# Kernel tuning notes

Measured on AMD Instinct MI355X. Metric: run time of the kernel, lower is better.

The kernel has to match this reference:

```python
import jax, jax.numpy as jnp
import numpy as np

FOCAL_ALPHA = 0.25
FOCAL_GAMMA = 2.0
LAMBDA_L1, LAMBDA_GIOU, LAMBDA_CONF = 1.0, 2.0, 1.0
IOU_THRESH = 0.3  # hardcoded `max_iou > 0.3` in assign_positives


def _make_boxes(key, shape):
    # valid xyxy boxes in [0,1]: random center + moderate size
    r = jax.random.uniform(key, shape + (4,), dtype=jnp.float32)
    cx = 0.1 + 0.8 * r[..., 0]
    cy = 0.1 + 0.8 * r[..., 1]
    w = 0.05 + 0.30 * r[..., 2]
    h = 0.05 + 0.30 * r[..., 3]
    return jnp.stack([cx - w / 2, cy - h / 2, cx + w / 2, cy + h / 2], axis=-1)


def setup_inputs() -> dict:
    key = jax.random.key(0)
    k1, k2, k3, k4, k5 = jax.random.split(key, 5)
    B, C, H, W, N = 16, 64, 80, 80, 32
    pred_boxes = _make_boxes(k1, (B, C, H, W))          # [B,C,H,W,4] xyxy
    confidences = jax.random.uniform(k2, (B, C, H, W), dtype=jnp.float32)
    cam = jax.random.uniform(k3, (B, C, H, W), dtype=jnp.float32)
    gt_boxes = _make_boxes(k4, (B, N))                   # [B,N,4] xyxy
    gt_labels = jax.random.randint(k5, (B, N), 0, C, dtype=jnp.int32)
    return {"pred_boxes": pred_boxes, "confidences": confidences, "cam": cam,
            "gt_boxes": gt_boxes, "gt_labels": gt_labels}


def box_giou(b1, b2):
    """Generalized IoU for xyxy boxes, broadcasting over leading dims."""
    a1 = (b1[..., 2] - b1[..., 0]) * (b1[..., 3] - b1[..., 1])
    a2 = (b2[..., 2] - b2[..., 0]) * (b2[..., 3] - b2[..., 1])
    lt = jnp.maximum(b1[..., :2], b2[..., :2])
    rb = jnp.minimum(b1[..., 2:], b2[..., 2:])
    wh = jnp.clip(rb - lt, 0.0)
    inter = wh[..., 0] * wh[..., 1]
    union = a1 + a2 - inter
    iou = inter / union
    lte = jnp.minimum(b1[..., :2], b2[..., :2])
    rbe = jnp.maximum(b1[..., 2:], b2[..., 2:])
    whe = jnp.clip(rbe - lte, 0.0)
    ae = whe[..., 0] * whe[..., 1]
    return iou - (ae - union) / ae


def _loss(pred_boxes, confidences, cam, gt_boxes, gt_labels):
    B, C, H, W, _ = pred_boxes.shape
    N = gt_boxes.shape[1]
    ii = jnp.arange(H)
    jj = jnp.arange(W)
    ch = jnp.arange(C)

    def assign_one(pb, gb, gl):  # pb [C,H,W,4], gb [N,4], gl [N]
        def step(carry, g):
            pos, matched = carry
            lab = gl[g]
            box = gb[g]
            pc = pb[lab].reshape(H * W, 4)
            giou = box_giou(pc, box[None, :])          # [H*W]
            idx = jnp.argmax(giou)
            valid = giou[idx] > IOU_THRESH
            mi, mj = idx // W, idx % W
            # pos_radius=1.5 -> window rows [mi-2, mi+1], cols [mj-2, mj+1]
            win = (((ii >= mi - 2) & (ii <= mi + 1))[:, None]
                   & ((jj >= mj - 2) & (jj <= mj + 1))[None, :])
            full = (ch == lab)[:, None, None] & (valid & win)[None]
            return (pos | full, jnp.where(full, g, matched)), None

        init = (jnp.zeros((C, H, W), bool), jnp.full((C, H, W), -1, jnp.int32))
        (pos, matched), _ = jax.lax.scan(step, init, jnp.arange(N))
        return pos, matched

    pos_mask, matched = jax.vmap(assign_one)(pred_boxes, gt_boxes, gt_labels)
    # gather matched gt box per position (later gts overwrite earlier, as in scan)
    gt_at = jax.vmap(lambda gb, m: gb[m])(gt_boxes, jnp.maximum(matched, 0))  # [B,C,H,W,4]

    l1 = jnp.mean(jnp.abs(pred_boxes - gt_at), axis=-1)   # F.l1_loss per pair
    giou_p = box_giou(pred_boxes, gt_at)
    num_pos = jnp.sum(pos_mask)
    denom = jnp.maximum(num_pos, 1).astype(jnp.float32)
    loss_l1 = jnp.sum(jnp.where(pos_mask, l1, 0.0)) / denom
    loss_giou = jnp.sum(jnp.where(pos_mask, 1.0 - giou_p, 0.0)) / denom

    conf_t = pos_mask.astype(jnp.float32)
    p = jnp.clip(confidences, 1e-6, 1.0 - 1e-6)
    ce = -(conf_t * jnp.log(p) + (1.0 - conf_t) * jnp.log1p(-p))
    p_t = p * conf_t + (1.0 - p) * (1.0 - conf_t)
    alpha_t = FOCAL_ALPHA * conf_t + (1.0 - FOCAL_ALPHA) * (1.0 - conf_t)
    loss_conf = jnp.mean(alpha_t * (1.0 - p_t) ** FOCAL_GAMMA * ce)

    loss_total = LAMBDA_L1 * loss_l1 + LAMBDA_GIOU * loss_giou + LAMBDA_CONF * loss_conf
    pos_ratio = num_pos.astype(jnp.float32) / (B * C * H * W)
    return loss_l1, loss_giou, loss_conf, loss_total, pos_ratio


@jax.jit
def reference(pred_boxes, confidences, cam, gt_boxes, gt_labels):
    return _loss(pred_boxes, confidences, cam, gt_boxes, gt_labels)
```

## Files before the change

### kernel.cpp

```cpp
#include <hip/hip_runtime.h>
#include <math.h>

constexpr int B = 16, C = 64, H = 80, Wd = 80, N = 32;
constexpr int HW = H * Wd;
constexpr int CHW = C * HW;
constexpr long long TOTAL = (long long)B * CHW;


constexpr int A_ITER = HW / 256;

__global__ __launch_bounds__(256) void assign_kernel(
    const float* __restrict__ pred,
    const float* __restrict__ gtb,
    const int*   __restrict__ gtl,
    int4* __restrict__ assign)
{
#pragma clang fp contract(off)
    const int bg = blockIdx.x;
    const int b = bg >> 5;
    const int g = bg & 31;
    const int tid = threadIdx.x;

    const int lab = gtl[b * N + g];
    const float4 gb = ((const float4*)gtb)[b * N + g];
    const float a2 = (gb.z - gb.x) * (gb.w - gb.y);

    const float4* pc = (const float4*)(pred + (size_t)(b * C + lab) * HW * 4);

    float4 buf[A_ITER];
#pragma unroll
    for (int k = 0; k < A_ITER; k++)
        buf[k] = pc[tid + k * 256];

    float best = -INFINITY;
    int bidx = 0x7fffffff;
#pragma unroll
    for (int k = 0; k < A_ITER; k++) {
        float4 pb = buf[k];
        float a1 = (pb.z - pb.x) * (pb.w - pb.y);
        float ltx = fmaxf(pb.x, gb.x), lty = fmaxf(pb.y, gb.y);
        float rbx = fminf(pb.z, gb.z), rby = fminf(pb.w, gb.w);
        float wx = fmaxf(rbx - ltx, 0.0f), wy = fmaxf(rby - lty, 0.0f);
        float inter = wx * wy;
        float uni = (a1 + a2) - inter;
        float iou = inter / uni;
        float lex = fminf(pb.x, gb.x), ley = fminf(pb.y, gb.y);
        float rex = fmaxf(pb.z, gb.z), rey = fmaxf(pb.w, gb.w);
        float ex = fmaxf(rex - lex, 0.0f), ey = fmaxf(rey - ley, 0.0f);
        float ae = ex * ey;
        float gi = iou - (ae - uni) / ae;
        if (gi > best) { best = gi; bidx = tid + k * 256; }
    }

    __shared__ float sv[256];
    __shared__ int   si[256];
    sv[tid] = best; si[tid] = bidx;
    __syncthreads();
    for (int s = 128; s > 0; s >>= 1) {
        if (tid < s) {
            float v2 = sv[tid + s]; int i2 = si[tid + s];
            float v1 = sv[tid];     int i1 = si[tid];
            if (v2 > v1 || (v2 == v1 && i2 < i1)) { sv[tid] = v2; si[tid] = i2; }
        }
        __syncthreads();
    }
    if (tid == 0) {
        int idx = si[0];
        float v = sv[0];
        int4 r;
        r.x = (v > 0.3f) ? 1 : 0;
        r.y = idx / Wd;
        r.z = idx % Wd;
        r.w = lab;
        assign[bg] = r;
    }
}

constexpr int K2_PER_THREAD = 16;
constexpr int K2_BLOCK_ELEMS = 256 * K2_PER_THREAD;
constexpr int K2_BLOCKS_PER_BATCH = CHW / K2_BLOCK_ELEMS;
constexpr int NBLK = B * K2_BLOCKS_PER_BATCH;

__global__ __launch_bounds__(256) void main_kernel(
    const float* __restrict__ pred,
    const float* __restrict__ conf,
    const float* __restrict__ gtb,
    const int4*  __restrict__ assign,
    float4* __restrict__ partials)
{
    const int tid = threadIdx.x;
    const int b = blockIdx.x / K2_BLOCKS_PER_BATCH;
    const int base = (blockIdx.x % K2_BLOCKS_PER_BATCH) * K2_BLOCK_ELEMS;
    const int pos0 = base + tid * K2_PER_THREAD;

    const float4* conf4 = (const float4*)(conf + (size_t)b * CHW);
    float4 q[4];
#pragma unroll
    for (int k = 0; k < 4; k++) q[k] = conf4[(pos0 >> 2) + k];

    const int c = pos0 / HW;
    const int rem = pos0 - c * HW;
    const int h = rem / Wd;
    const int w0 = rem - h * Wd;

    __shared__ int s_cnt;
    __shared__ int4 s_gt[N];
    if (tid == 0) s_cnt = 0;
    __syncthreads();
    const int c0 = base / HW;
    const int c1 = (base + K2_BLOCK_ELEMS - 1) / HW;
    if (tid < N) {
        int4 a = assign[b * N + tid];
        if (a.x && a.w >= c0 && a.w <= c1) {
            int k = atomicAdd(&s_cnt, 1);
            s_gt[k] = make_int4(tid, a.w, a.y, a.z);
        }
    }
    __syncthreads();
    const int cnt = s_cnt;

    int m[K2_PER_THREAD];
#pragma unroll
    for (int e = 0; e < K2_PER_THREAD; e++) m[e] = -1;
    for (int j = 0; j < cnt; j++) {
        int4 a = s_gt[j];
        if (a.y == c && h >= a.z - 2 && h <= a.z + 1) {
#pragma unroll
            for (int e = 0; e < K2_PER_THREAD; e++) {
                int w = w0 + e;
                if (w >= a.w - 2 && w <= a.w + 1) m[e] = max(m[e], a.x);
            }
        }
    }

    float pv[K2_PER_THREAD];
#pragma unroll
    for (int k = 0; k < 4; k++) {
        pv[4 * k + 0] = q[k].x; pv[4 * k + 1] = q[k].y;
        pv[4 * k + 2] = q[k].z; pv[4 * k + 3] = q[k].w;
    }

    float l_l1 = 0.0f, l_gi = 0.0f, l_f = 0.0f, l_np = 0.0f;

#pragma unroll
    for (int e = 0; e < K2_PER_THREAD; e++) {
        float p = fminf(fmaxf(pv[e], 1e-6f), 1.0f - 1e-6f);
        if (m[e] >= 0) {
#pragma clang fp contract(off)
            float om = 1.0f - p;
            l_f += 0.25f * om * om * (-logf(p));
            l_np += 1.0f;

            int pos = pos0 + e;
            float4 pb = *(const float4*)(pred + ((size_t)b * CHW + pos) * 4);
            float4 gb = ((const float4*)gtb)[b * N + m[e]];
            l_l1 += 0.25f * (fabsf(pb.x - gb.x) + fabsf(pb.y - gb.y) +
                             fabsf(pb.z - gb.z) + fabsf(pb.w - gb.w));

            float a1 = (pb.z - pb.x) * (pb.w - pb.y);
            float a2 = (gb.z - gb.x) * (gb.w - gb.y);
            float ltx = fmaxf(pb.x, gb.x), lty = fmaxf(pb.y, gb.y);
            float rbx = fminf(pb.z, gb.z), rby = fminf(pb.w, gb.w);
            float wx = fmaxf(rbx - ltx, 0.0f), wy = fmaxf(rby - lty, 0.0f);
            float inter = wx * wy;
            float uni = (a1 + a2) - inter;
            float iou = inter / uni;
            float lex = fminf(pb.x, gb.x), ley = fminf(pb.y, gb.y);
            float rex = fmaxf(pb.z, gb.z), rey = fmaxf(pb.w, gb.w);
            float ex = fmaxf(rex - lex, 0.0f), ey = fmaxf(rey - ley, 0.0f);
            float ae = ex * ey;
            float gi = iou - (ae - uni) / ae;
            l_gi += 1.0f - gi;
        } else {
            l_f += 0.75f * p * p * (-log1pf(-p));
        }
    }

    __shared__ float r0[256], r1[256], r2[256], r3[256];
    r0[tid] = l_l1; r1[tid] = l_gi; r2[tid] = l_f; r3[tid] = l_np;
    __syncthreads();
    for (int s = 128; s > 0; s >>= 1) {
        if (tid < s) {
            r0[tid] += r0[tid + s];
            r1[tid] += r1[tid + s];
            r2[tid] += r2[tid + s];
            r3[tid] += r3[tid + s];
        }
        __syncthreads();
    }
    if (tid == 0)
        partials[blockIdx.x] = make_float4(r0[0], r1[0], r2[0], r3[0]);
}

__global__ __launch_bounds__(256) void final_kernel(
    const float4* __restrict__ partials,
    float* __restrict__ out)
{
    const int tid = threadIdx.x;
    float s0 = 0.0f, s1 = 0.0f, s2 = 0.0f, s3 = 0.0f;
    for (int i = tid; i < NBLK; i += 256) {
        float4 p = partials[i];
        s0 += p.x; s1 += p.y; s2 += p.z; s3 += p.w;
    }
    __shared__ float r0[256], r1[256], r2[256], r3[256];
    r0[tid] = s0; r1[tid] = s1; r2[tid] = s2; r3[tid] = s3;
    __syncthreads();
    for (int s = 128; s > 0; s >>= 1) {
        if (tid < s) {
            r0[tid] += r0[tid + s];
            r1[tid] += r1[tid + s];
            r2[tid] += r2[tid + s];
            r3[tid] += r3[tid + s];
        }
        __syncthreads();
    }
    if (tid == 0) {
        float np = r3[0];
        float denom = fmaxf(np, 1.0f);
        float l1 = r0[0] / denom;
        float gi = r1[0] / denom;
        float cf = r2[0] / (float)TOTAL;
        out[0] = l1;
        out[1] = gi;
        out[2] = cf;
        out[3] = l1 + 2.0f * gi + cf;
        out[4] = np / (float)TOTAL;
    }
}

extern "C" void kernel_launch(void* const* d_in, const int* in_sizes, int n_in,
                              void* d_out, int out_size, void* d_ws, size_t ws_size,
                              hipStream_t stream) {
    const float* pred = (const float*)d_in[0];
    const float* conf = (const float*)d_in[1];
    const float* gtb  = (const float*)d_in[3];
    const int*   gtl  = (const int*)d_in[4];

    int4*   assign   = (int4*)d_ws;
    float4* partials = (float4*)((char*)d_ws + 8192);
    float*  out      = (float*)d_out;

    assign_kernel<<<B * N, 256, 0, stream>>>(pred, gtb, gtl, assign);
    main_kernel<<<NBLK, 256, 0, stream>>>(pred, conf, gtb, assign, partials);
    final_kernel<<<1, 256, 0, stream>>>(partials, out);
}
```

Baseline: 210.8 us.

## Split per-GT argmax over spatial chunks and use fast log intrinsics

The assignment kernel now splits each ground-truth's argmax over H*W into 5 chunks, launching five times as many blocks, each holding fewer registers of buffered boxes. It writes partial (value, index) pairs that the main kernel combines with lowest-index tie-breaking. The aim is more parallelism and occupancy in the assignment phase, which previously ran only 512 blocks with 25 float4 loads per thread. The focal loss also switches to the __logf intrinsic in place of logf and log1pf, which may cost a little accuracy for p near 0.

```diff
diff --git a/kernel.cpp b/kernel.cpp
--- a/kernel.cpp
+++ b/kernel.cpp
@@ -6,36 +6,40 @@
 constexpr int CHW = C * HW;
 constexpr long long TOTAL = (long long)B * CHW;
 
-
-constexpr int A_ITER = HW / 256;
-
-__global__ __launch_bounds__(256) void assign_kernel(
+constexpr int NCHUNK = 5;
+constexpr int CHUNK_ELEMS = HW / NCHUNK;
+constexpr int A_DEPTH = CHUNK_ELEMS / 256;
+
+
+__global__ __launch_bounds__(256) void assign_partial_kernel(
     const float* __restrict__ pred,
     const float* __restrict__ gtb,
     const int*   __restrict__ gtl,
-    int4* __restrict__ assign)
+    int2* __restrict__ amax)
 {
 #pragma clang fp contract(off)
-    const int bg = blockIdx.x;
+    const int blk = blockIdx.x;
+    const int bg = blk / NCHUNK;
+    const int chunk = blk - bg * NCHUNK;
     const int b = bg >> 5;
-    const int g = bg & 31;
     const int tid = threadIdx.x;
 
-    const int lab = gtl[b * N + g];
-    const float4 gb = ((const float4*)gtb)[b * N + g];
+    const int lab = gtl[bg];
+    const float4 gb = ((const float4*)gtb)[bg];
     const float a2 = (gb.z - gb.x) * (gb.w - gb.y);
 
-    const float4* pc = (const float4*)(pred + (size_t)(b * C + lab) * HW * 4);
-
-    float4 buf[A_ITER];
-#pragma unroll
-    for (int k = 0; k < A_ITER; k++)
+    const float4* pc = (const float4*)(pred + (size_t)(b * C + lab) * HW * 4)
+                       + chunk * CHUNK_ELEMS;
+
+    float4 buf[A_DEPTH];
+#pragma unroll
+    for (int k = 0; k < A_DEPTH; k++)
         buf[k] = pc[tid + k * 256];
 
     float best = -INFINITY;
     int bidx = 0x7fffffff;
 #pragma unroll
-    for (int k = 0; k < A_ITER; k++) {
+    for (int k = 0; k < A_DEPTH; k++) {
         float4 pb = buf[k];
         float a1 = (pb.z - pb.x) * (pb.w - pb.y);
         float ltx = fmaxf(pb.x, gb.x), lty = fmaxf(pb.y, gb.y);
@@ -49,7 +53,7 @@
         float ex = fmaxf(rex - lex, 0.0f), ey = fmaxf(rey - ley, 0.0f);
         float ae = ex * ey;
         float gi = iou - (ae - uni) / ae;
-        if (gi > best) { best = gi; bidx = tid + k * 256; }
+        if (gi > best) { best = gi; bidx = chunk * CHUNK_ELEMS + tid + k * 256; }
     }
 
     __shared__ float sv[256];
@@ -59,21 +63,14 @@
     for (int s = 128; s > 0; s >>= 1) {
         if (tid < s) {
             float v2 = sv[tid + s]; int i2 = si[tid + s];
-            float v1 = sv[tid];     int i1 = si[tid];
-            if (v2 > v1 || (v2 == v1 && i2 < i1)) { sv[tid] = v2; si[tid] = i2; }
+            if (v2 > sv[tid] || (v2 == sv[tid] && i2 < si[tid])) {
+                sv[tid] = v2; si[tid] = i2;
+            }
         }
         __syncthreads();
     }
-    if (tid == 0) {
-        int idx = si[0];
-        float v = sv[0];
-        int4 r;
-        r.x = (v > 0.3f) ? 1 : 0;
-        r.y = idx / Wd;
-        r.z = idx % Wd;
-        r.w = lab;
-        assign[bg] = r;
-    }
+    if (tid == 0)
+        amax[blk] = make_int2(__float_as_int(sv[0]), si[0]);
 }
 
 constexpr int K2_PER_THREAD = 16;
@@ -85,7 +82,8 @@
     const float* __restrict__ pred,
     const float* __restrict__ conf,
     const float* __restrict__ gtb,
-    const int4*  __restrict__ assign,
+    const int*   __restrict__ gtl,
+    const int2*  __restrict__ amax,
     float4* __restrict__ partials)
 {
     const int tid = threadIdx.x;
@@ -110,10 +108,21 @@
     const int c0 = base / HW;
     const int c1 = (base + K2_BLOCK_ELEMS - 1) / HW;
     if (tid < N) {
-        int4 a = assign[b * N + tid];
-        if (a.x && a.w >= c0 && a.w <= c1) {
-            int k = atomicAdd(&s_cnt, 1);
-            s_gt[k] = make_int4(tid, a.w, a.y, a.z);
+        const int bg = b * N + tid;
+        float best = -INFINITY;
+        int idx = 0x7fffffff;
+#pragma unroll
+        for (int kc = 0; kc < NCHUNK; kc++) {
+            int2 pr = amax[bg * NCHUNK + kc];
+            float v = __int_as_float(pr.x);
+            if (v > best || (v == best && pr.y < idx)) { best = v; idx = pr.y; }
+        }
+        if (best > 0.3f) {
+            int lab = gtl[bg];
+            if (lab >= c0 && lab <= c1) {
+                int k = atomicAdd(&s_cnt, 1);
+                s_gt[k] = make_int4(tid, lab, idx / Wd, idx % Wd);
+            }
         }
     }
     __syncthreads();
@@ -148,7 +157,7 @@
         if (m[e] >= 0) {
 #pragma clang fp contract(off)
             float om = 1.0f - p;
-            l_f += 0.25f * om * om * (-logf(p));
+            l_f += 0.25f * om * om * (-__logf(p));
             l_np += 1.0f;
 
             int pos = pos0 + e;
@@ -172,7 +181,7 @@
             float gi = iou - (ae - uni) / ae;
             l_gi += 1.0f - gi;
         } else {
-            l_f += 0.75f * p * p * (-log1pf(-p));
+            l_f += 0.75f * p * p * (-__logf(1.0f - p));
         }
     }
 
@@ -236,11 +245,11 @@
     const float* gtb  = (const float*)d_in[3];
     const int*   gtl  = (const int*)d_in[4];
 
-    int4*   assign   = (int4*)d_ws;
-    float4* partials = (float4*)((char*)d_ws + 8192);
+    int2*   amax     = (int2*)d_ws;
+    float4* partials = (float4*)((char*)d_ws + 32768);
     float*  out      = (float*)d_out;
 
-    assign_kernel<<<B * N, 256, 0, stream>>>(pred, gtb, gtl, assign);
-    main_kernel<<<NBLK, 256, 0, stream>>>(pred, conf, gtb, assign, partials);
+    assign_partial_kernel<<<B * N * NCHUNK, 256, 0, stream>>>(pred, gtb, gtl, amax);
+    main_kernel<<<NBLK, 256, 0, stream>>>(pred, conf, gtb, gtl, amax, partials);
     final_kernel<<<1, 256, 0, stream>>>(partials, out);
 }
```

Result: faster. 190.1 us (-9.8%).
